# Kernel optimization log

Hardware: AMD Instinct MI355X
Metric: run time of the kernel (lower is better)

The kernel has to match this reference:

```python
import jax, jax.numpy as jnp
import numpy as np
from jax import lax

N, T, CH, EMB, H, C = 256, 87, 21, 50, 128, 43  # utterances, max tokens, chars, glove dim, gru hidden, classes


def setup_inputs() -> dict:
    key = jax.random.key(0)
    ks = iter(jax.random.split(key, 40))
    def rn(shape, s=0.1):
        return (jax.random.normal(next(ks), shape) * s).astype(jnp.float32)
    return {
        "token_embeddings": rn((N, T, EMB), 1.0),
        "token_char_embeddings": rn((N, T, CH, EMB), 1.0),
        "conv1_w": rn((T, T, 5, 5)), "conv1_b": rn((T,)),
        "conv2_w": rn((T, T, 5, 5)), "conv2_b": rn((T,)),
        "utt_wih_f": rn((3 * H, 58)), "utt_whh_f": rn((3 * H, H)),
        "utt_bih_f": rn((3 * H,)), "utt_bhh_f": rn((3 * H,)),
        "utt_wih_b": rn((3 * H, 58)), "utt_whh_b": rn((3 * H, H)),
        "utt_bih_b": rn((3 * H,)), "utt_bhh_b": rn((3 * H,)),
        "ctx_w1": rn((H, 2 * H)), "ctx_w2": rn((H, H)), "ctx_b2": rn((H,)), "ctx_w3": rn((H, H)),
        "proj_w": rn((1, 2 * H)), "proj_b": rn((1,)),
        "gx0": rn((2, 2, H)),
        "cg_wih_f": rn((3 * H, 1)), "cg_whh_f": rn((3 * H, H)),
        "cg_bih_f": rn((3 * H,)), "cg_bhh_f": rn((3 * H,)),
        "cg_wih_b": rn((3 * H, 1)), "cg_whh_b": rn((3 * H, H)),
        "cg_bih_b": rn((3 * H,)), "cg_bhh_b": rn((3 * H,)),
        "cls_w1": rn((2 * H, 4 * H)), "cls_b1": rn((2 * H,)),
        "cls_w2": rn((H, 2 * H)), "cls_b2": rn((H,)),
        "cls_w3": rn((C, H)), "cls_b3": rn((C,)),
    }


def gru_cell(x, h, wih, whh, bih, bhh):
    # torch nn.GRU gate order: r, z, n
    gi = x @ wih.T + bih
    gh = h @ whh.T + bhh
    ir, iz, in_ = jnp.split(gi, 3, axis=-1)
    hr, hz, hn = jnp.split(gh, 3, axis=-1)
    r = jax.nn.sigmoid(ir + hr)
    z = jax.nn.sigmoid(iz + hz)
    n = jnp.tanh(in_ + r * hn)
    return (1.0 - z) * n + z * h


def gru_last(x_tbd, h0, wih, whh, bih, bhh):
    # x_tbd: [T, B, D] time-major; returns final hidden [B, H]
    def step(h, xt):
        return gru_cell(xt, h, wih, whh, bih, bhh), None
    hT, _ = lax.scan(step, h0, x_tbd)
    return hT


def _forward(token_embeddings, token_char_embeddings, conv1_w, conv1_b, conv2_w, conv2_b,
             utt_wih_f, utt_whh_f, utt_bih_f, utt_bhh_f,
             utt_wih_b, utt_whh_b, utt_bih_b, utt_bhh_b,
             ctx_w1, ctx_w2, ctx_b2, ctx_w3, proj_w, proj_b, gx0,
             cg_wih_f, cg_whh_f, cg_bih_f, cg_bhh_f,
             cg_wih_b, cg_whh_b, cg_bih_b, cg_bhh_b,
             cls_w1, cls_b1, cls_w2, cls_b2, cls_w3, cls_b3):
    def conv(x, w, b):
        y = lax.conv_general_dilated(x, w, (1, 1), 'VALID',
                                     dimension_numbers=('NCHW', 'OIHW', 'NCHW'))
        return y + b[None, :, None, None]

    def maxpool(x):
        return lax.reduce_window(x, -jnp.inf, lax.max, (1, 1, 3, 3), (1, 1, 2, 2), 'VALID')

    # utterance CNN over char embeddings: [N,87,21,50] -> [N,87,1,8]
    x = maxpool(jax.nn.relu(conv(token_char_embeddings, conv1_w, conv1_b)))
    x = maxpool(jax.nn.relu(conv(x, conv2_w, conv2_b)))
    cnn = x.reshape(x.shape[0], x.shape[1], -1)  # [N,87,8]
    rnn_in = jnp.concatenate([token_embeddings, cnn], axis=2)  # [N,87,58]

    # bidirectional utterance GRU -> final hidden states, [N,256]
    x_tm = jnp.swapaxes(rnn_in, 0, 1)  # [87,N,58]
    h0 = jnp.zeros((rnn_in.shape[0], H), dtype=rnn_in.dtype)
    hf = gru_last(x_tm, h0, utt_wih_f, utt_whh_f, utt_bih_f, utt_bhh_f)
    hb = gru_last(x_tm[::-1], h0, utt_wih_b, utt_whh_b, utt_bih_b, utt_bhh_b)
    Hall = jnp.concatenate([hf, hb], axis=1)  # [N,256]

    def conv_gru(seq, hx):
        # seq: [2,128,1] (batch=2, seq=128, feat=1); hx: [2,2,128] (dir, batch, hid)
        stm = jnp.swapaxes(seq, 0, 1)  # [128,2,1]
        hf_ = gru_last(stm, hx[0], cg_wih_f, cg_whh_f, cg_bih_f, cg_bhh_f)
        hb_ = gru_last(stm[::-1], hx[1], cg_wih_b, cg_whh_b, cg_bih_b, cg_bhh_b)
        return jnp.stack([hf_, hb_])  # [2,2,128]

    def ctx_step(gx, hx_row):
        gx_sg = lax.stop_gradient(gx)  # matches .detach() in the original
        Hx = hx_row[None, :]                        # [1,256]
        a = Hx @ ctx_w1.T                           # [1,128]
        b = gx_sg[0][:, None, :] @ ctx_w2.T + ctx_b2  # [2,1,128]
        S = jnp.tanh(a + b) @ ctx_w3.T              # [2,1,128]
        A = jax.nn.softmax(S, axis=-1)              # [2,1,128]
        Mx = A[:, 0, :, None] * Hx[0][None, None, :]  # A^T @ Hx -> [2,128,256]
        one_d = Mx @ proj_w.T + proj_b              # [2,128,1]
        new_gx = conv_gru(one_d, gx_sg)             # [2,2,128]
        return new_gx, new_gx.reshape(-1)           # feature = gx.view(1,-1) -> 512

    _, feats = lax.scan(ctx_step, gx0, Hall)  # [N,512]

    h1 = jax.nn.leaky_relu(feats @ cls_w1.T + cls_b1)
    h2 = jax.nn.leaky_relu(h1 @ cls_w2.T + cls_b2)
    return h2 @ cls_w3.T + cls_b3  # [N,43]


def reference(token_embeddings, token_char_embeddings, conv1_w, conv1_b, conv2_w, conv2_b,
              utt_wih_f, utt_whh_f, utt_bih_f, utt_bhh_f,
              utt_wih_b, utt_whh_b, utt_bih_b, utt_bhh_b,
              ctx_w1, ctx_w2, ctx_b2, ctx_w3, proj_w, proj_b, gx0,
              cg_wih_f, cg_whh_f, cg_bih_f, cg_bhh_f,
              cg_wih_b, cg_whh_b, cg_bih_b, cg_bhh_b,
              cls_w1, cls_b1, cls_w2, cls_b2, cls_w3, cls_b3):
    return _forward(token_embeddings, token_char_embeddings, conv1_w, conv1_b, conv2_w, conv2_b,
                    utt_wih_f, utt_whh_f, utt_bih_f, utt_bhh_f,
                    utt_wih_b, utt_whh_b, utt_bih_b, utt_bhh_b,
                    ctx_w1, ctx_w2, ctx_b2, ctx_w3, proj_w, proj_b, gx0,
                    cg_wih_f, cg_whh_f, cg_bih_f, cg_bhh_f,
                    cg_wih_b, cg_whh_b, cg_bih_b, cg_bhh_b,
                    cls_w1, cls_b1, cls_w2, cls_b2, cls_w3, cls_b3)
```

## Files before the change

kernel.cpp:

```cpp
#include <hip/hip_runtime.h>
#include <math.h>

#define NB   256
#define TDIM 87
#define HD   128
#define H3   384
#define NCLS 43

typedef float f32x4 __attribute__((ext_vector_type(4)));
typedef _Float16 f16x8 __attribute__((ext_vector_type(8)));
typedef _Float16 f16x2 __attribute__((ext_vector_type(2)));

__device__ __forceinline__ float sigmoidf_(float x){ return 1.0f/(1.0f + __expf(-x)); }
__device__ __forceinline__ float tanhf_(float x){ return 1.0f - 2.0f/(1.0f + __expf(2.0f*x)); }
__device__ __forceinline__ float lrelu_(float x){ return x > 0.f ? x : 0.01f*x; }

__device__ __forceinline__ f32x4 gload4(const float* p_){
  f32x4 r;
  asm volatile("global_load_dwordx4 %0, %1, off" : "=v"(r) : "v"(p_));
  return r;
}
__device__ __forceinline__ float dot4v(float acc, f32x4 a, f32x4 b){
  acc = fmaf(a[0], b[0], acc); acc = fmaf(a[1], b[1], acc);
  acc = fmaf(a[2], b[2], acc); acc = fmaf(a[3], b[3], acc);
  return acc;
}
__device__ __forceinline__ float dot8h(float acc, f16x8 a, f16x8 b){
  acc = __builtin_amdgcn_fdot2(__builtin_shufflevector(a,a,0,1), __builtin_shufflevector(b,b,0,1), acc, false);
  acc = __builtin_amdgcn_fdot2(__builtin_shufflevector(a,a,2,3), __builtin_shufflevector(b,b,2,3), acc, false);
  acc = __builtin_amdgcn_fdot2(__builtin_shufflevector(a,a,4,5), __builtin_shufflevector(b,b,4,5), acc, false);
  acc = __builtin_amdgcn_fdot2(__builtin_shufflevector(a,a,6,7), __builtin_shufflevector(b,b,6,7), acc, false);
  return acc;
}
__device__ __forceinline__ f16x8 cvt8h(const float* p){
  f16x8 r;
  #pragma unroll
  for (int j=0;j<8;j++) r[j] = (_Float16)p[j];
  return r;
}
__device__ __forceinline__ void h8tof(f16x8 a, f32x4& lo, f32x4& hi){
  lo[0]=(float)a[0]; lo[1]=(float)a[1]; lo[2]=(float)a[2]; lo[3]=(float)a[3];
  hi[0]=(float)a[4]; hi[1]=(float)a[5]; hi[2]=(float)a[6]; hi[3]=(float)a[7];
}

__global__ __launch_bounds__(256) void k_conv1(const float* __restrict__ tce,
    const float* __restrict__ w1, const float* __restrict__ b1,
    float* __restrict__ pool1){
  const int n = blockIdx.x, oc = blockIdx.y;
  __shared__ float xs[21*52];
  __shared__ float ws[32];
  __shared__ float cv[17*48];
  const int tid = threadIdx.x;
  const int oh = tid/12, owc = (tid%12)*4;
  const bool act = tid < 204;
  const float bias = b1[oc];
  float acc[4];
  #pragma unroll
  for (int j=0;j<4;j++) acc[j] = bias;
  const float* xin  = tce + (size_t)(n*TDIM)*1050;
  const float* wrow = w1  + (size_t)oc*TDIM*25;
  for (int ic=0; ic<TDIM; ++ic){
    for (int j=tid; j<1050; j+=256){ xs[(j/50)*52 + (j%50)] = xin[(size_t)ic*1050 + j]; }
    if (tid < 25) ws[tid] = wrow[ic*25 + tid];
    __syncthreads();
    if (act){
      float wreg[25];
      #pragma unroll
      for (int u=0;u<25;u++) wreg[u] = ws[u];
      #pragma unroll
      for (int r=0;r<5;r++){
        const float4* xr = (const float4*)&xs[(oh+r)*52 + owc];
        float4 v0 = xr[0], v1 = xr[1];
        float xv[8] = {v0.x,v0.y,v0.z,v0.w,v1.x,v1.y,v1.z,v1.w};
        #pragma unroll
        for (int c=0;c<5;c++){
          float w = wreg[r*5+c];
          #pragma unroll
          for (int j=0;j<4;j++) acc[j] = fmaf(w, xv[c+j], acc[j]);
        }
      }
    }
    __syncthreads();
  }
  if (act){
    #pragma unroll
    for (int j=0;j<4;j++){
      int ow = owc + j;
      if (ow < 46) cv[oh*48 + ow] = fmaxf(acc[j], 0.0f);
    }
  }
  __syncthreads();
  if (tid < 176){
    int ph = tid/22, pw = tid%22;
    float m = -1e30f;
    #pragma unroll
    for (int r=0;r<3;r++)
      #pragma unroll
      for (int c=0;c<3;c++)
        m = fmaxf(m, cv[(2*ph+r)*48 + (2*pw+c)]);
    pool1[((size_t)(n*TDIM+oc))*176 + tid] = m;
  }
}

__global__ __launch_bounds__(128) void k_conv2(const float* __restrict__ pool1,
    const float* __restrict__ w2, const float* __restrict__ b2,
    float* __restrict__ cnn){
  const int n = blockIdx.x, oc = blockIdx.y;
  __shared__ float xs[176];
  __shared__ float ws[32];
  __shared__ float cv[72];
  const int tid = threadIdx.x;
  float a = b2[oc];
  const int oh = tid/18, ow = tid%18;
  const float* xin = pool1 + (size_t)n*TDIM*176;
  const float* wr  = w2 + (size_t)oc*TDIM*25;
  for (int ic=0; ic<TDIM; ++ic){
    for (int j=tid; j<176; j+=128) xs[j] = xin[(size_t)ic*176 + j];
    if (tid < 25) ws[tid] = wr[ic*25 + tid];
    __syncthreads();
    if (tid < 72){
      #pragma unroll
      for (int r=0;r<5;r++)
        #pragma unroll
        for (int c=0;c<5;c++)
          a = fmaf(ws[r*5+c], xs[(oh+r)*22 + (ow+c)], a);
    }
    __syncthreads();
  }
  if (tid < 72) cv[tid] = fmaxf(a, 0.0f);
  __syncthreads();
  if (tid < 8){
    float m = -1e30f;
    #pragma unroll
    for (int r=0;r<3;r++)
      #pragma unroll
      for (int c=0;c<3;c++)
        m = fmaxf(m, cv[r*18 + (2*tid+c)]);
    cnn[((size_t)(n*TDIM+oc))*8 + tid] = m;
  }
}

__global__ __launch_bounds__(768,3) void k_utt(
    const float* __restrict__ te, const float* __restrict__ cnn,
    const float* __restrict__ wih_f, const float* __restrict__ whh_f,
    const float* __restrict__ bih_f, const float* __restrict__ bhh_f,
    const float* __restrict__ wih_b, const float* __restrict__ whh_b,
    const float* __restrict__ bih_b, const float* __restrict__ bhh_b,
    float* __restrict__ Hall){
  const int bx  = blockIdx.x;
  const int dir = bx & 1;
  const int n   = bx >> 1;
  const int tid = threadIdx.x;
  const int o   = tid >> 1, kh = tid & 1;
  const float* wih = dir ? wih_b : wih_f;
  const float* whh = dir ? whh_b : whh_f;
  const float* bih = dir ? bih_b : bih_f;
  const float* bhh = dir ? bhh_b : bhh_f;
  float wh[64], wi[32];
  { const float4* wp = (const float4*)(whh + (size_t)o*128 + kh*64);
    #pragma unroll
    for (int q=0;q<16;q++){ float4 v=wp[q]; wh[4*q]=v.x; wh[4*q+1]=v.y; wh[4*q+2]=v.z; wh[4*q+3]=v.w; } }
  #pragma unroll
  for (int k=0;k<32;k++){ int c = kh*32 + k; wi[k] = (c < 58) ? wih[(size_t)o*58 + c] : 0.f; }
  const float bI = bih[o], bH = bhh[o];
  __shared__ float h[128];
  __shared__ float xb[64];
  __shared__ float s_rz[256];
  __shared__ float gin_s[128];
  __shared__ float ghn_s[128];
  if (tid < 128) h[tid] = 0.f;
  if (tid < 64)  xb[tid] = 0.f;
  __syncthreads();
  for (int t=0;t<TDIM;++t){
    const int ttt = dir ? (TDIM-1-t) : t;
    if (tid < 50)      xb[tid] = te[((size_t)n*TDIM + ttt)*50 + tid];
    else if (tid < 58) xb[tid] = cnn[((size_t)n*TDIM + ttt)*8 + (tid - 50)];
    __syncthreads();
    float a0=0,a1=0,a2=0,a3=0;
    const float4* hp = (const float4*)&h[kh*64];
    #pragma unroll
    for (int q=0;q<16;q++){ float4 hv=hp[q];
      a0=fmaf(wh[4*q],hv.x,a0); a1=fmaf(wh[4*q+1],hv.y,a1);
      a2=fmaf(wh[4*q+2],hv.z,a2); a3=fmaf(wh[4*q+3],hv.w,a3); }
    float ah = (a0+a1)+(a2+a3);
    float c0=0,c1=0,c2=0,c3=0;
    const float4* xp = (const float4*)&xb[kh*32];
    #pragma unroll
    for (int q=0;q<8;q++){ float4 xv=xp[q];
      c0=fmaf(wi[4*q],xv.x,c0); c1=fmaf(wi[4*q+1],xv.y,c1);
      c2=fmaf(wi[4*q+2],xv.z,c2); c3=fmaf(wi[4*q+3],xv.w,c3); }
    float ai = (c0+c1)+(c2+c3);
    ah += __shfl_xor(ah, 1);
    ai += __shfl_xor(ai, 1);
    if (kh == 0){
      if (o < 256) s_rz[o] = ah + ai + bI + bH;
      else { gin_s[o-256] = ai + bI; ghn_s[o-256] = ah + bH; }
    }
    __syncthreads();
    if (tid < 128){
      float r  = sigmoidf_(s_rz[tid]);
      float z  = sigmoidf_(s_rz[128+tid]);
      float nn = tanhf_(gin_s[tid] + r*ghn_s[tid]);
      h[tid] = (1.f - z)*nn + z*h[tid];
    }
    __syncthreads();
  }
  if (tid < 128) Hall[(size_t)n*256 + dir*128 + tid] = h[tid];
}

__global__ __launch_bounds__(256) void k_prep(const float* __restrict__ Hall,
    const float* __restrict__ ctx_w1, const float* __restrict__ proj_w,
    float* __restrict__ a_all, float* __restrict__ s_all){
  const int i = blockIdx.x; const int tid = threadIdx.x;
  __shared__ float hr[256];
  __shared__ float red[2];
  hr[tid] = Hall[(size_t)i*256 + tid];
  __syncthreads();
  if (tid < 128){
    const float4* w  = (const float4*)(ctx_w1 + (size_t)tid*256);
    const float4* hp = (const float4*)hr;
    float a0=0,a1=0,a2=0,a3=0;
    #pragma unroll 8
    for (int q=0;q<64;q++){ float4 wv=w[q], hv=hp[q];
      a0=fmaf(wv.x,hv.x,a0); a1=fmaf(wv.y,hv.y,a1); a2=fmaf(wv.z,hv.z,a2); a3=fmaf(wv.w,hv.w,a3); }
    a_all[(size_t)i*128 + tid] = (a0+a1)+(a2+a3);
  } else {
    const int k = tid - 128;
    float p = hr[k]*proj_w[k] + hr[k+128]*proj_w[k+128];
    #pragma unroll
    for (int off=32; off; off>>=1) p += __shfl_xor(p, off);
    if ((tid & 63) == 0) red[(tid-128)>>6] = p;
  }
  __syncthreads();
  if (tid == 0) s_all[i] = red[0] + red[1];
}

__global__ __launch_bounds__(512,2) void k_ctx(
    const float* __restrict__ cg_wih_f, const float* __restrict__ cg_whh_f,
    const float* __restrict__ cg_bih_f, const float* __restrict__ cg_bhh_f,
    const float* __restrict__ cg_wih_b, const float* __restrict__ cg_whh_b,
    const float* __restrict__ cg_bih_b, const float* __restrict__ cg_bhh_b,
    const float* __restrict__ ctx_w2, const float* __restrict__ ctx_b2,
    const float* __restrict__ ctx_w3, const float* __restrict__ proj_b,
    const float* __restrict__ gx0,
    const float* __restrict__ a_all, const float* __restrict__ s_all,
    float* __restrict__ one_d_g, int* __restrict__ flags,
    float* __restrict__ feats){
  const int blk = blockIdx.x;
  const bool isF = blk < 2;
  const int d   = blk & 1;
  const int tid = threadIdx.x;
  const int p   = tid >> 2;
  const int kq  = tid & 3;
  const float* whh = isF ? cg_whh_f : cg_whh_b;
  const float* wih = isF ? cg_wih_f : cg_wih_b;
  const float* bih = isF ? cg_bih_f : cg_bih_b;
  const float* bhh = isF ? cg_bhh_f : cg_bhh_b;

  const float* wrb = whh + (size_t)(      p)*128 + kq*32;
  const float* wzb = whh + (size_t)(128 + p)*128 + kq*32;
  const float* wnb = whh + (size_t)(256 + p)*128 + kq*32;
  f16x8 wr0=cvt8h(wrb), wr1=cvt8h(wrb+8), wr2=cvt8h(wrb+16), wr3=cvt8h(wrb+24);
  f16x8 wz0=cvt8h(wzb), wz1=cvt8h(wzb+8), wz2=cvt8h(wzb+16), wz3=cvt8h(wzb+24);
  f16x8 wn0=cvt8h(wnb), wn1=cvt8h(wnb+8), wn2=cvt8h(wnb+16), wn3=cvt8h(wnb+24);
  asm volatile("" : "+v"(wr0), "+v"(wr1), "+v"(wr2), "+v"(wr3),
                    "+v"(wz0), "+v"(wz1), "+v"(wz2), "+v"(wz3),
                    "+v"(wn0), "+v"(wn1), "+v"(wn2), "+v"(wn3));

  float wir = wih[p],      wiz = wih[128+p], win = wih[256+p];
  float br_ = bih[p]      + bhh[p];
  float bz_ = bih[128+p]  + bhh[128+p];
  float bn_ = bih[256+p];
  float bhn_ = bhh[256+p];
  float pb = proj_b[0];
  asm volatile("" : "+v"(wir), "+v"(wiz), "+v"(win), "+v"(br_), "+v"(bz_),
                    "+v"(bn_), "+v"(bhn_), "+v"(pb));

  __shared__ _Float16 hl16[2][160];
  __shared__ float one_d_s[128];
  __shared__ float T_s[160];
  __shared__ float S_s[128];
  __shared__ float red_s[2];

  const float* gsrc = gx0 + (size_t)((isF ? 0 : 2) + d)*128;
  float hm = gsrc[p];
  if (tid < 128) hl16[0][((tid>>5)*40) + (tid&31)] = (_Float16)gsrc[tid];
  __syncthreads();

  const int chp  = ((p>>5)*40) + (p&31);
  const int kb16 = kq*40;

  for (int i=0;i<NB;++i){
    if (isF){
      const float* w2r = ctx_w2 + (size_t)p*128 + kq*32;
      const float* w3r = ctx_w3 + (size_t)p*128 + kq*32;
      f32x4 u0=gload4(w2r),    u1=gload4(w2r+4),  u2=gload4(w2r+8),  u3=gload4(w2r+12);
      f32x4 u4=gload4(w2r+16), u5=gload4(w2r+20), u6=gload4(w2r+24), u7=gload4(w2r+28);
      f32x4 v0=gload4(w3r),    v1=gload4(w3r+4),  v2=gload4(w3r+8),  v3=gload4(w3r+12);
      f32x4 v4=gload4(w3r+16), v5=gload4(w3r+20), v6=gload4(w3r+24), v7=gload4(w3r+28);
      asm volatile("s_waitcnt vmcnt(0)" ::: "memory");
      __builtin_amdgcn_sched_barrier(0);
      {
        const f16x8* hp0 = (const f16x8*)&hl16[0][kb16];
        f16x8 a0=hp0[0], a1=hp0[1], a2=hp0[2], a3=hp0[3];
        f32x4 g0,g1,g2,g3,g4,g5,g6,g7;
        h8tof(a0,g0,g1); h8tof(a1,g2,g3); h8tof(a2,g4,g5); h8tof(a3,g6,g7);
        float s=0;
        s=dot4v(s,u0,g0); s=dot4v(s,u1,g1); s=dot4v(s,u2,g2); s=dot4v(s,u3,g3);
        s=dot4v(s,u4,g4); s=dot4v(s,u5,g5); s=dot4v(s,u6,g6); s=dot4v(s,u7,g7);
        s += __shfl_xor(s,1); s += __shfl_xor(s,2);
        if (kq == 0) T_s[((p>>4)*20)+(p&15)] = tanhf_(a_all[(size_t)i*128 + p] + s + ctx_b2[p]);
      }
      __syncthreads();
      {
        const f32x4* tA = (const f32x4*)&T_s[kq*40];
        const f32x4* tB = (const f32x4*)&T_s[kq*40+20];
        f32x4 t0=tA[0],t1=tA[1],t2=tA[2],t3=tA[3];
        f32x4 t4=tB[0],t5=tB[1],t6=tB[2],t7=tB[3];
        float s=0;
        s=dot4v(s,v0,t0); s=dot4v(s,v1,t1); s=dot4v(s,v2,t2); s=dot4v(s,v3,t3);
        s=dot4v(s,v4,t4); s=dot4v(s,v5,t5); s=dot4v(s,v6,t6); s=dot4v(s,v7,t7);
        s += __shfl_xor(s,1); s += __shfl_xor(s,2);
        if (kq == 0) S_s[p] = s;
      }
      __syncthreads();
      if (tid < 64){
        float m = fmaxf(S_s[tid], S_s[tid+64]);
        #pragma unroll
        for (int off=32; off; off>>=1) m = fmaxf(m, __shfl_xor(m, off));
        if (tid == 0) red_s[0] = m;
      }
      __syncthreads();
      if (tid < 128) S_s[tid] = __expf(S_s[tid] - red_s[0]);
      __syncthreads();
      if (tid < 64){
        float s = S_s[tid] + S_s[tid+64];
        #pragma unroll
        for (int off=32; off; off>>=1) s += __shfl_xor(s, off);
        if (tid == 0) red_s[1] = s;
      }
      __syncthreads();
      if (tid < 128){
        float v = (S_s[tid] / red_s[1]) * s_all[i] + pb;
        one_d_s[tid] = v;
        __hip_atomic_store(&one_d_g[((size_t)d*NB + i)*128 + tid], v,
                           __ATOMIC_RELAXED, __HIP_MEMORY_SCOPE_AGENT);
      }
      __syncthreads();
      if (tid == 0){
        __threadfence();
        __hip_atomic_store(&flags[d], i+1, __ATOMIC_RELEASE, __HIP_MEMORY_SCOPE_AGENT);
      }
    } else {
      if (tid == 0){
        while (__hip_atomic_load(&flags[d], __ATOMIC_ACQUIRE, __HIP_MEMORY_SCOPE_AGENT) < i+1){
          __builtin_amdgcn_s_sleep(8);
        }
      }
      __syncthreads();
      if (tid < 128)
        one_d_s[tid] = __hip_atomic_load(&one_d_g[((size_t)d*NB + i)*128 + tid],
                                         __ATOMIC_RELAXED, __HIP_MEMORY_SCOPE_AGENT);
      __syncthreads();
    }
    for (int tc=0; tc<128; ++tc){
      const _Float16* hcur = hl16[tc & 1];
      _Float16*       hnxt = hl16[(tc & 1) ^ 1];
      const f16x8* hp = (const f16x8*)&hcur[kb16];
      f16x8 h0=hp[0], h1=hp[1], h2=hp[2], h3=hp[3];
      float ar=0, az=0, an=0;
      ar=dot8h(ar,wr0,h0); ar=dot8h(ar,wr1,h1); ar=dot8h(ar,wr2,h2); ar=dot8h(ar,wr3,h3);
      az=dot8h(az,wz0,h0); az=dot8h(az,wz1,h1); az=dot8h(az,wz2,h2); az=dot8h(az,wz3,h3);
      an=dot8h(an,wn0,h0); an=dot8h(an,wn1,h1); an=dot8h(an,wn2,h2); an=dot8h(an,wn3,h3);
      ar += __shfl_xor(ar,1); ar += __shfl_xor(ar,2);
      az += __shfl_xor(az,1); az += __shfl_xor(az,2);
      an += __shfl_xor(an,1); an += __shfl_xor(an,2);
      if (kq == 0){
        float x = one_d_s[isF ? tc : 127-tc];
        float r  = sigmoidf_(fmaf(x, wir, br_) + ar);
        float z  = sigmoidf_(fmaf(x, wiz, bz_) + az);
        float nn = tanhf_(fmaf(x, win, bn_) + r*(an + bhn_));
        hm = (1.f - z)*nn + z*hm;
        hnxt[chp] = (_Float16)hm;
      }
      __syncthreads();
    }
    if (kq == 0){
      const int off = isF ? d*128 : 256 + d*128;
      feats[(size_t)i*512 + off + p] = hm;
    }
    __syncthreads();
  }
}

__global__ __launch_bounds__(256) void k_cls(const float* __restrict__ feats,
    const float* __restrict__ w1, const float* __restrict__ b1,
    const float* __restrict__ w2, const float* __restrict__ b2,
    const float* __restrict__ w3, const float* __restrict__ b3,
    float* __restrict__ out){
  const int n = blockIdx.x; const int tid = threadIdx.x;
  __shared__ float fr[512];
  __shared__ float h1s[256];
  __shared__ float h2s[128];
  fr[tid]       = feats[(size_t)n*512 + tid];
  fr[tid+256]   = feats[(size_t)n*512 + 256 + tid];
  __syncthreads();
  {
    const float4* w  = (const float4*)(w1 + (size_t)tid*512);
    const float4* fp = (const float4*)fr;
    float a0=0,a1=0,a2=0,a3=0;
    #pragma unroll 8
    for (int q=0;q<128;q++){ float4 wv=w[q], fv=fp[q];
      a0=fmaf(wv.x,fv.x,a0); a1=fmaf(wv.y,fv.y,a1); a2=fmaf(wv.z,fv.z,a2); a3=fmaf(wv.w,fv.w,a3); }
    h1s[tid] = lrelu_(b1[tid] + (a0+a1)+(a2+a3));
  }
  __syncthreads();
  if (tid < 128){
    const float4* w  = (const float4*)(w2 + (size_t)tid*256);
    const float4* fp = (const float4*)h1s;
    float a0=0,a1=0,a2=0,a3=0;
    #pragma unroll 8
    for (int q=0;q<64;q++){ float4 wv=w[q], fv=fp[q];
      a0=fmaf(wv.x,fv.x,a0); a1=fmaf(wv.y,fv.y,a1); a2=fmaf(wv.z,fv.z,a2); a3=fmaf(wv.w,fv.w,a3); }
    h2s[tid] = lrelu_(b2[tid] + (a0+a1)+(a2+a3));
  }
  __syncthreads();
  if (tid < NCLS){
    const float4* w  = (const float4*)(w3 + (size_t)tid*128);
    const float4* fp = (const float4*)h2s;
    float a0=0,a1=0,a2=0,a3=0;
    #pragma unroll 8
    for (int q=0;q<32;q++){ float4 wv=w[q], fv=fp[q];
      a0=fmaf(wv.x,fv.x,a0); a1=fmaf(wv.y,fv.y,a1); a2=fmaf(wv.z,fv.z,a2); a3=fmaf(wv.w,fv.w,a3); }
    out[(size_t)n*NCLS + tid] = b3[tid] + (a0+a1)+(a2+a3);
  }
}

#define OFF_FLAGS  0u
#define OFF_SALL   512u
#define OFF_AALL   2048u
#define OFF_ONED   133632u
#define OFF_HALL   395776u
#define OFF_FEATS  657920u
#define OFF_CNN    1182208u
#define OFF_POOL1  1894912u

extern "C" void kernel_launch(void* const* d_in, const int* in_sizes, int n_in,
                              void* d_out, int out_size, void* d_ws, size_t ws_size,
                              hipStream_t stream){
  const float* te   = (const float*)d_in[0];
  const float* tce  = (const float*)d_in[1];
  const float* c1w  = (const float*)d_in[2];
  const float* c1b  = (const float*)d_in[3];
  const float* c2w  = (const float*)d_in[4];
  const float* c2b  = (const float*)d_in[5];
  const float* uwif = (const float*)d_in[6];
  const float* uwhf = (const float*)d_in[7];
  const float* ubif = (const float*)d_in[8];
  const float* ubhf = (const float*)d_in[9];
  const float* uwib = (const float*)d_in[10];
  const float* uwhb = (const float*)d_in[11];
  const float* ubib = (const float*)d_in[12];
  const float* ubhb = (const float*)d_in[13];
  const float* cw1  = (const float*)d_in[14];
  const float* cw2  = (const float*)d_in[15];
  const float* cb2  = (const float*)d_in[16];
  const float* cw3  = (const float*)d_in[17];
  const float* pw   = (const float*)d_in[18];
  const float* pbb  = (const float*)d_in[19];
  const float* gx0  = (const float*)d_in[20];
  const float* gwif = (const float*)d_in[21];
  const float* gwhf = (const float*)d_in[22];
  const float* gbif = (const float*)d_in[23];
  const float* gbhf = (const float*)d_in[24];
  const float* gwib = (const float*)d_in[25];
  const float* gwhb = (const float*)d_in[26];
  const float* gbib = (const float*)d_in[27];
  const float* gbhb = (const float*)d_in[28];
  const float* clw1 = (const float*)d_in[29];
  const float* clb1 = (const float*)d_in[30];
  const float* clw2 = (const float*)d_in[31];
  const float* clb2 = (const float*)d_in[32];
  const float* clw3 = (const float*)d_in[33];
  const float* clb3 = (const float*)d_in[34];
  float* out = (float*)d_out;
  char* ws = (char*)d_ws;
  int*   flags = (int*)  (ws + OFF_FLAGS);
  float* s_all = (float*)(ws + OFF_SALL);
  float* a_all = (float*)(ws + OFF_AALL);
  float* one_d = (float*)(ws + OFF_ONED);
  float* Hall  = (float*)(ws + OFF_HALL);
  float* feats = (float*)(ws + OFF_FEATS);
  float* cnn   = (float*)(ws + OFF_CNN);
  float* pool1 = (float*)(ws + OFF_POOL1);

  hipMemsetAsync(flags, 0, 64, stream);
  k_conv1<<<dim3(NB, TDIM), 256, 0, stream>>>(tce, c1w, c1b, pool1);
  k_conv2<<<dim3(NB, TDIM), 128, 0, stream>>>(pool1, c2w, c2b, cnn);
  k_utt<<<512, 768, 0, stream>>>(te, cnn, uwif, uwhf, ubif, ubhf,
                                 uwib, uwhb, ubib, ubhb, Hall);
  k_prep<<<NB, 256, 0, stream>>>(Hall, cw1, pw, a_all, s_all);
  k_ctx<<<4, 512, 0, stream>>>(gwif, gwhf, gbif, gbhf, gwib, gwhb, gbib, gbhb,
                               cw2, cb2, cw3, pbb, gx0, a_all, s_all,
                               one_d, flags, feats);
  k_cls<<<NB, 256, 0, stream>>>(feats, clw1, clb1, clw2, clb2, clw3, clb3, out);
}
```

Before: 22.71 ms.

## Merge the two context GRU chains per direction into one 1024-thread block

```diff
diff --git a/kernel.cpp b/kernel.cpp
--- a/kernel.cpp
+++ b/kernel.cpp
@@ -235,7 +235,7 @@
   if (tid == 0) s_all[i] = red[0] + red[1];
 }
 
-__global__ __launch_bounds__(512,2) void k_ctx(
+__global__ __launch_bounds__(1024,1) void k_ctx(
     const float* __restrict__ cg_wih_f, const float* __restrict__ cg_whh_f,
     const float* __restrict__ cg_bih_f, const float* __restrict__ cg_bhh_f,
     const float* __restrict__ cg_wih_b, const float* __restrict__ cg_whh_b,
@@ -246,12 +246,12 @@
     const float* __restrict__ a_all, const float* __restrict__ s_all,
     float* __restrict__ one_d_g, int* __restrict__ flags,
     float* __restrict__ feats){
-  const int blk = blockIdx.x;
-  const bool isF = blk < 2;
-  const int d   = blk & 1;
+  const bool isF = (blockIdx.x == 0);
   const int tid = threadIdx.x;
-  const int p   = tid >> 2;
-  const int kq  = tid & 3;
+  const int ch  = tid >> 9;
+  const int lt  = tid & 511;
+  const int p   = lt >> 2;
+  const int kq  = lt & 3;
   const float* whh = isF ? cg_whh_f : cg_whh_b;
   const float* wih = isF ? cg_wih_f : cg_wih_b;
   const float* bih = isF ? cg_bih_f : cg_bih_b;
@@ -276,15 +276,15 @@
   asm volatile("" : "+v"(wir), "+v"(wiz), "+v"(win), "+v"(br_), "+v"(bz_),
                     "+v"(bn_), "+v"(bhn_), "+v"(pb));
 
-  __shared__ _Float16 hl16[2][160];
-  __shared__ float one_d_s[128];
-  __shared__ float T_s[160];
-  __shared__ float S_s[128];
-  __shared__ float red_s[2];
-
-  const float* gsrc = gx0 + (size_t)((isF ? 0 : 2) + d)*128;
+  __shared__ _Float16 hl16[2][2][160];
+  __shared__ float one_d_s[2][128];
+  __shared__ float T_s[2][160];
+  __shared__ float S_s[2][128];
+  __shared__ float red_s[2][2];
+
+  const float* gsrc = gx0 + (size_t)((isF ? 0 : 2) + ch)*128;
   float hm = gsrc[p];
-  if (tid < 128) hl16[0][((tid>>5)*40) + (tid&31)] = (_Float16)gsrc[tid];
+  if (lt < 128) hl16[ch][0][((lt>>5)*40) + (lt&31)] = (_Float16)gsrc[lt];
   __syncthreads();
 
   const int chp  = ((p>>5)*40) + (p&31);
@@ -301,7 +301,7 @@
       asm volatile("s_waitcnt vmcnt(0)" ::: "memory");
       __builtin_amdgcn_sched_barrier(0);
       {
-        const f16x8* hp0 = (const f16x8*)&hl16[0][kb16];
+        const f16x8* hp0 = (const f16x8*)&hl16[ch][0][kb16];
         f16x8 a0=hp0[0], a1=hp0[1], a2=hp0[2], a3=hp0[3];
         f32x4 g0,g1,g2,g3,g4,g5,g6,g7;
         h8tof(a0,g0,g1); h8tof(a1,g2,g3); h8tof(a2,g4,g5); h8tof(a3,g6,g7);
@@ -309,63 +309,63 @@
         s=dot4v(s,u0,g0); s=dot4v(s,u1,g1); s=dot4v(s,u2,g2); s=dot4v(s,u3,g3);
         s=dot4v(s,u4,g4); s=dot4v(s,u5,g5); s=dot4v(s,u6,g6); s=dot4v(s,u7,g7);
         s += __shfl_xor(s,1); s += __shfl_xor(s,2);
-        if (kq == 0) T_s[((p>>4)*20)+(p&15)] = tanhf_(a_all[(size_t)i*128 + p] + s + ctx_b2[p]);
+        if (kq == 0) T_s[ch][((p>>4)*20)+(p&15)] = tanhf_(a_all[(size_t)i*128 + p] + s + ctx_b2[p]);
       }
       __syncthreads();
       {
-        const f32x4* tA = (const f32x4*)&T_s[kq*40];
-        const f32x4* tB = (const f32x4*)&T_s[kq*40+20];
+        const f32x4* tA = (const f32x4*)&T_s[ch][kq*40];
+        const f32x4* tB = (const f32x4*)&T_s[ch][kq*40+20];
         f32x4 t0=tA[0],t1=tA[1],t2=tA[2],t3=tA[3];
         f32x4 t4=tB[0],t5=tB[1],t6=tB[2],t7=tB[3];
         float s=0;
         s=dot4v(s,v0,t0); s=dot4v(s,v1,t1); s=dot4v(s,v2,t2); s=dot4v(s,v3,t3);
         s=dot4v(s,v4,t4); s=dot4v(s,v5,t5); s=dot4v(s,v6,t6); s=dot4v(s,v7,t7);
         s += __shfl_xor(s,1); s += __shfl_xor(s,2);
-        if (kq == 0) S_s[p] = s;
-      }
-      __syncthreads();
-      if (tid < 64){
-        float m = fmaxf(S_s[tid], S_s[tid+64]);
+        if (kq == 0) S_s[ch][p] = s;
+      }
+      __syncthreads();
+      if (lt < 64){
+        float m = fmaxf(S_s[ch][lt], S_s[ch][lt+64]);
         #pragma unroll
         for (int off=32; off; off>>=1) m = fmaxf(m, __shfl_xor(m, off));
-        if (tid == 0) red_s[0] = m;
-      }
-      __syncthreads();
-      if (tid < 128) S_s[tid] = __expf(S_s[tid] - red_s[0]);
-      __syncthreads();
-      if (tid < 64){
-        float s = S_s[tid] + S_s[tid+64];
+        if (lt == 0) red_s[ch][0] = m;
+      }
+      __syncthreads();
+      if (lt < 128) S_s[ch][lt] = __expf(S_s[ch][lt] - red_s[ch][0]);
+      __syncthreads();
+      if (lt < 64){
+        float s = S_s[ch][lt] + S_s[ch][lt+64];
         #pragma unroll
         for (int off=32; off; off>>=1) s += __shfl_xor(s, off);
-        if (tid == 0) red_s[1] = s;
-      }
-      __syncthreads();
-      if (tid < 128){
-        float v = (S_s[tid] / red_s[1]) * s_all[i] + pb;
-        one_d_s[tid] = v;
-        __hip_atomic_store(&one_d_g[((size_t)d*NB + i)*128 + tid], v,
+        if (lt == 0) red_s[ch][1] = s;
+      }
+      __syncthreads();
+      if (lt < 128){
+        float v = (S_s[ch][lt] / red_s[ch][1]) * s_all[i] + pb;
+        one_d_s[ch][lt] = v;
+        __hip_atomic_store(&one_d_g[((size_t)ch*NB + i)*128 + lt], v,
                            __ATOMIC_RELAXED, __HIP_MEMORY_SCOPE_AGENT);
       }
       __syncthreads();
       if (tid == 0){
         __threadfence();
-        __hip_atomic_store(&flags[d], i+1, __ATOMIC_RELEASE, __HIP_MEMORY_SCOPE_AGENT);
+        __hip_atomic_store(&flags[0], i+1, __ATOMIC_RELEASE, __HIP_MEMORY_SCOPE_AGENT);
       }
     } else {
       if (tid == 0){
-        while (__hip_atomic_load(&flags[d], __ATOMIC_ACQUIRE, __HIP_MEMORY_SCOPE_AGENT) < i+1){
+        while (__hip_atomic_load(&flags[0], __ATOMIC_ACQUIRE, __HIP_MEMORY_SCOPE_AGENT) < i+1){
           __builtin_amdgcn_s_sleep(8);
         }
       }
       __syncthreads();
-      if (tid < 128)
-        one_d_s[tid] = __hip_atomic_load(&one_d_g[((size_t)d*NB + i)*128 + tid],
-                                         __ATOMIC_RELAXED, __HIP_MEMORY_SCOPE_AGENT);
+      if (lt < 128)
+        one_d_s[ch][lt] = __hip_atomic_load(&one_d_g[((size_t)ch*NB + i)*128 + lt],
+                                            __ATOMIC_RELAXED, __HIP_MEMORY_SCOPE_AGENT);
       __syncthreads();
     }
     for (int tc=0; tc<128; ++tc){
-      const _Float16* hcur = hl16[tc & 1];
-      _Float16*       hnxt = hl16[(tc & 1) ^ 1];
+      const _Float16* hcur = hl16[ch][tc & 1];
+      _Float16*       hnxt = hl16[ch][(tc & 1) ^ 1];
       const f16x8* hp = (const f16x8*)&hcur[kb16];
       f16x8 h0=hp[0], h1=hp[1], h2=hp[2], h3=hp[3];
       float ar=0, az=0, an=0;
@@ -376,7 +376,7 @@
       az += __shfl_xor(az,1); az += __shfl_xor(az,2);
       an += __shfl_xor(an,1); an += __shfl_xor(an,2);
       if (kq == 0){
-        float x = one_d_s[isF ? tc : 127-tc];
+        float x = one_d_s[ch][isF ? tc : 127-tc];
         float r  = sigmoidf_(fmaf(x, wir, br_) + ar);
         float z  = sigmoidf_(fmaf(x, wiz, bz_) + az);
         float nn = tanhf_(fmaf(x, win, bn_) + r*(an + bhn_));
@@ -386,7 +386,7 @@
       __syncthreads();
     }
     if (kq == 0){
-      const int off = isF ? d*128 : 256 + d*128;
+      const int off = isF ? ch*128 : 256 + ch*128;
       feats[(size_t)i*512 + off + p] = hm;
     }
     __syncthreads();
@@ -500,8 +500,8 @@
   k_utt<<<512, 768, 0, stream>>>(te, cnn, uwif, uwhf, ubif, ubhf,
                                  uwib, uwhb, ubib, ubhb, Hall);
   k_prep<<<NB, 256, 0, stream>>>(Hall, cw1, pw, a_all, s_all);
-  k_ctx<<<4, 512, 0, stream>>>(gwif, gwhf, gbif, gbhf, gwib, gwhb, gbib, gbhb,
-                               cw2, cb2, cw3, pbb, gx0, a_all, s_all,
-                               one_d, flags, feats);
+  k_ctx<<<2, 1024, 0, stream>>>(gwif, gwhf, gbif, gbhf, gwib, gwhb, gbib, gbhb,
+                                cw2, cb2, cw3, pbb, gx0, a_all, s_all,
+                                one_d, flags, feats);
   k_cls<<<NB, 256, 0, stream>>>(feats, clw1, clb1, clw2, clb2, clw3, clb3, out);
 }
```

After: 43.51 ms. 91.6% more time.
